# Optimization experiments

Hardware: AMD Instinct MI355X
Metric: run time of the kernel (lower is better)

Reference implementation:

```python
import jax, jax.numpy as jnp
import numpy as np

DEPTH, HEADS, DIM, DH = 6, 3, 3, 128
INNER = HEADS * DH            # 384
M = int(DH * np.log(DH))      # 620 random features (performer_pytorch default)
FF = 4 * DIM                  # 12
EPS = 1e-4


def setup_inputs() -> dict:
    key = jax.random.key(0)
    ks = jax.random.split(key, 12)
    B, N = 8, 4096
    s = 0.1
    return {
        "x": jax.random.normal(ks[0], (B, N, DIM), jnp.float32),
        "Wq": jax.random.normal(ks[1], (DEPTH, DIM, INNER), jnp.float32) * s,
        "Wk": jax.random.normal(ks[2], (DEPTH, DIM, INNER), jnp.float32) * s,
        "Wv": jax.random.normal(ks[3], (DEPTH, DIM, INNER), jnp.float32) * s,
        "Wo": jax.random.normal(ks[4], (DEPTH, INNER, DIM), jnp.float32) * s,
        "bo": jnp.zeros((DEPTH, DIM), jnp.float32),
        "ln1_g": jnp.ones((DEPTH, DIM), jnp.float32),
        "ln1_b": jnp.zeros((DEPTH, DIM), jnp.float32),
        "W1": jax.random.normal(ks[5], (DEPTH, DIM, FF), jnp.float32) * s,
        "b1": jnp.zeros((DEPTH, FF), jnp.float32),
        "W2": jax.random.normal(ks[6], (DEPTH, FF, DIM), jnp.float32) * s,
        "b2": jnp.zeros((DEPTH, DIM), jnp.float32),
        "ln2_g": jnp.ones((DEPTH, DIM), jnp.float32),
        "ln2_b": jnp.zeros((DEPTH, DIM), jnp.float32),
        "proj": jax.random.normal(ks[7], (DEPTH, M, DH), jnp.float32),
        "dec_w": jax.random.normal(ks[8], (DIM, 1), jnp.float32) * s,
        "dec_b": jnp.zeros((1,), jnp.float32),
    }


def layernorm(x, g, b):
    mu = x.mean(-1, keepdims=True)
    var = ((x - mu) ** 2).mean(-1, keepdims=True)
    return (x - mu) * jax.lax.rsqrt(var + 1e-5) * g + b


def softmax_kernel(data, proj, is_query):
    # data: [b,h,n,dh], proj: [m,dh] -> positive random features [b,h,n,m]
    dn = DH ** -0.25                    # data normalizer 1/sqrt(sqrt(d))
    ratio = M ** -0.5
    dd = jnp.einsum('bhnd,md->bhnm', data * dn, proj)
    diag = 0.5 * (dn ** 2) * (data ** 2).sum(-1, keepdims=True)  # [b,h,n,1]
    if is_query:
        mx = jnp.max(dd, axis=-1, keepdims=True)
    else:
        mx = jnp.max(dd, axis=(-1, -2), keepdims=True)
    return ratio * (jnp.exp(dd - diag - mx) + EPS)


def favor_attention(x, Wq, Wk, Wv, Wo, bo, proj):
    b, n, _ = x.shape
    split = lambda t: t.reshape(b, n, HEADS, DH).transpose(0, 2, 1, 3)
    q, k, v = split(x @ Wq), split(x @ Wk), split(x @ Wv)   # [b,h,n,dh]
    qp = softmax_kernel(q, proj, True)    # [b,h,n,m]
    kp = softmax_kernel(k, proj, False)
    k_sum = kp.sum(axis=2)                                   # [b,h,m]
    d_inv = 1.0 / jnp.einsum('bhnm,bhm->bhn', qp, k_sum)
    ctx = jnp.einsum('bhnm,bhnd->bhmd', kp, v)               # [b,h,m,dh]
    out = jnp.einsum('bhnm,bhmd,bhn->bhnd', qp, ctx, d_inv)
    out = out.transpose(0, 2, 1, 3).reshape(b, n, INNER)
    return out @ Wo + bo


def reference(x, Wq, Wk, Wv, Wo, bo, ln1_g, ln1_b, W1, b1, W2, b2, ln2_g, ln2_b, proj, dec_w, dec_b):
    for i in range(DEPTH):
        h = layernorm(x, ln1_g[i], ln1_b[i])
        x = x + favor_attention(h, Wq[i], Wk[i], Wv[i], Wo[i], bo[i], proj[i])
        h = layernorm(x, ln2_g[i], ln2_b[i])
        x = x + (jax.nn.gelu(h @ W1[i] + b1[i], approximate=False) @ W2[i] + b2[i])
    return jax.nn.sigmoid(x @ dec_w + dec_b)
```

## Files before the change

kernel.cpp:

```cpp
#include <hip/hip_runtime.h>
#include <math.h>

#define B_ 8
#define N_ 4096
#define H_ 3
#define DH_ 128
#define INNER_ 384
#define M_ 620
#define MP_ 640
#define DEPTH_ 6
#define BH_ 24

static constexpr float DN_ = 0.29730177875068026f;
static constexpr float RATIO_ = 0.04016096644512494f;
static constexpr float EPS_ = 1e-4f;

typedef __attribute__((ext_vector_type(8))) short short8;
typedef __attribute__((ext_vector_type(4))) float f32x4;

__device__ __forceinline__ short f2bf(float f) {
  union { float f; unsigned u; } x; x.f = f;
  unsigned r = x.u + 0x7FFF + ((x.u >> 16) & 1);
  return (short)(r >> 16);
}
__device__ __forceinline__ float bf2f(short s) {
  union { unsigned u; float f; } x; x.u = ((unsigned)(unsigned short)s) << 16;
  return x.f;
}
__device__ __forceinline__ float4 ldg4(const float* p) { return *(const float4*)p; }

__device__ __forceinline__ unsigned cvtpk(float lo, float hi) {
  unsigned r;
  asm("v_cvt_pk_bf16_f32 %0, %1, %2" : "=v"(r) : "v"(lo), "v"(hi));
  return r;
}

__device__ __forceinline__ void gl2lds(const void* g, void* l) {
  __builtin_amdgcn_global_load_lds(
      (const __attribute__((address_space(1))) void*)g,
      (__attribute__((address_space(3))) void*)l, 16, 0, 0);
}

__device__ __forceinline__ void stage_t256(const char* gbase, char* lds, int w, int l) {
  int row = w * 4 + (l >> 4);
  int col = ((l & 15) * 16) ^ ((row & 7) << 4);
  char* lp = lds + __builtin_amdgcn_readfirstlane(w << 10);
  gl2lds(gbase + row * 256 + col, lp);
}

__device__ __forceinline__ void stage_t64(const char* gbase, size_t growb, char* lds,
                                          int w, int l) {
  int d = w * 16 + (l >> 2);
  int swl = ((((l >> 2) ^ (l >> 4)) & 3) << 4);
  int col = ((l & 3) * 16) ^ swl;
  char* lp = lds + __builtin_amdgcn_readfirstlane(w << 10);
  gl2lds(gbase + (size_t)d * growb + col, lp);
}

__global__ void k_copy(const float* __restrict__ s, float* __restrict__ d, int n) {
  int i = blockIdx.x * 256 + threadIdx.x;
  if (i < n) d[i] = s[i];
}

__global__ void k_projcvt(const float* __restrict__ proj, short* __restrict__ pb) {
  int i = blockIdx.x * 256 + threadIdx.x;
  if (i >= DEPTH_ * MP_ * DH_) return;
  int l = i / (MP_ * DH_);
  int rem = i - l * (MP_ * DH_);
  int m = rem >> 7, d = rem & 127;
  pb[i] = (m < M_) ? f2bf(proj[((size_t)l * M_ + m) * DH_ + d]) : (short)0;
}

__global__ __launch_bounds__(384) void k_ln_qkv(
    const float* __restrict__ x, const float* __restrict__ Wq,
    const float* __restrict__ Wk, const float* __restrict__ Wv,
    const float* __restrict__ g1, const float* __restrict__ b1,
    short* __restrict__ qb, short* __restrict__ kb, short* __restrict__ vtp) {
  __shared__ float xs[96];
  int c = threadIdx.x;
  int token0 = blockIdx.x * 32;
  int b = token0 >> 12, n0 = token0 & 4095;
  if (c < 96) xs[c] = x[(size_t)token0 * 3 + c];
  float wq0 = Wq[c], wq1 = Wq[INNER_ + c], wq2 = Wq[2 * INNER_ + c];
  float wk0 = Wk[c], wk1 = Wk[INNER_ + c], wk2 = Wk[2 * INNER_ + c];
  float wv0 = Wv[c], wv1 = Wv[INNER_ + c], wv2 = Wv[2 * INNER_ + c];
  float G0 = g1[0], G1 = g1[1], G2 = g1[2];
  float B0 = b1[0], B1 = b1[1], B2 = b1[2];
  int hh = c >> 7, dh = c & 127;
  size_t rowbase = ((size_t)(b * H_ + hh) * N_ + n0) * DH_ + dh;
  __syncthreads();
  short8 v8[4];
#pragma unroll
  for (int tt = 0; tt < 32; ++tt) {
    float x0 = xs[tt * 3], x1 = xs[tt * 3 + 1], x2 = xs[tt * 3 + 2];
    float mu = (x0 + x1 + x2) * (1.f / 3.f);
    float d0 = x0 - mu, d1 = x1 - mu, d2 = x2 - mu;
    float rs = rsqrtf((d0 * d0 + d1 * d1 + d2 * d2) * (1.f / 3.f) + 1e-5f);
    float h0 = d0 * rs * G0 + B0;
    float h1 = d1 * rs * G1 + B1;
    float h2 = d2 * rs * G2 + B2;
    qb[rowbase + (size_t)tt * DH_] = f2bf((h0 * wq0 + h1 * wq1 + h2 * wq2) * DN_);
    kb[rowbase + (size_t)tt * DH_] = f2bf((h0 * wk0 + h1 * wk1 + h2 * wk2) * DN_);
    const int p = ((tt >> 2) & 3) * 8 + ((tt >> 4) & 1) * 4 + (tt & 3);
    v8[p >> 3][p & 7] = f2bf(h0 * wv0 + h1 * wv1 + h2 * wv2);
  }
  short* dst = vtp + ((size_t)(b * H_ + hh) * DH_ + dh) * N_ + n0;
  *(short8*)dst = v8[0];
  *(short8*)(dst + 8) = v8[1];
  *(short8*)(dst + 16) = v8[2];
  *(short8*)(dst + 24) = v8[3];
}

__global__ __launch_bounds__(256) void k_dv(
    const short* __restrict__ kb, const short* __restrict__ vtp,
    float* __restrict__ diag_k, float* __restrict__ vsp) {
  __shared__ float red[256];
  int xx = blockIdx.x, bh = blockIdx.y, t = threadIdx.x;
  if (xx < 128) {
    int d = xx;
    const short8* row = (const short8*)(vtp + ((size_t)bh * DH_ + d) * N_);
    short8 a = row[t * 2], b2 = row[t * 2 + 1];
    float s = 0.f;
#pragma unroll
    for (int j = 0; j < 8; ++j) s += bf2f(a[j]) + bf2f(b2[j]);
    red[t] = s;
    __syncthreads();
    for (int st = 128; st; st >>= 1) {
      if (t < st) red[t] += red[t + st];
      __syncthreads();
    }
    if (t == 0) vsp[bh * DH_ + d] = red[0];
  } else {
    int nt = xx - 128;
    int n = t >> 3, seg = t & 7;
    const short* src = kb + ((size_t)bh * N_ + nt * 32 + n) * DH_ + seg * 16;
    short8 a = *(const short8*)src;
    short8 b2 = *(const short8*)(src + 8);
    float s = 0.f;
#pragma unroll
    for (int j = 0; j < 8; ++j) {
      float va = bf2f(a[j]), vb = bf2f(b2[j]);
      s = fmaf(va, va, s);
      s = fmaf(vb, vb, s);
    }
    s += __shfl_down(s, 4);
    s += __shfl_down(s, 2);
    s += __shfl_down(s, 1);
    if (seg == 0) diag_k[(size_t)bh * N_ + nt * 32 + n] = 0.5f * s;
  }
}

__global__ __launch_bounds__(512) void k_kp_ctx(
    const short* __restrict__ kb, const short* __restrict__ vtp,
    const short* __restrict__ pb, const float* __restrict__ diag_k,
    float* __restrict__ Cpart, float* __restrict__ spart,
    float* __restrict__ bmx) {
  int ns = blockIdx.x, mt = blockIdx.y, bh = blockIdx.z;
  __shared__ __align__(16) char Ks[2][16384];
  __shared__ __align__(16) char Vts[2][16384];
  __shared__ float diag_s[1024];
  int t = threadIdx.x, w = t >> 6, l = t & 63, lr = l & 15, lg = l >> 4;
  {
    const float* dbase = diag_k + (size_t)bh * N_ + ns * 1024;
#pragma unroll
    for (int i = 0; i < 2; ++i) diag_s[t + i * 512] = dbase[t + i * 512];
  }
  int m0 = mt * 128 + w * 16;
  short8 bfr[4];
  {
    const short* pr = pb + (size_t)(m0 + lr) * DH_ + lg * 8;
#pragma unroll
    for (int ks = 0; ks < 4; ++ks) bfr[ks] = *(const short8*)(pr + ks * 32);
  }
  const char* kgb = (const char*)(kb + ((size_t)bh * N_ + ns * 1024) * DH_);
  const char* vgb = (const char*)(vtp + (size_t)bh * DH_ * N_ + ns * 1024);
  stage_t256(kgb, Ks[0], w, l);
  stage_t256(kgb + 32 * 256, Ks[0] + 8192, w, l);
  stage_t64(vgb, (size_t)N_ * 2, Vts[0], w, l);
  stage_t64(vgb + 64, (size_t)N_ * 2, Vts[0] + 8192, w, l);
  __syncthreads();
  f32x4 cacc[8];
#pragma unroll
  for (int db = 0; db < 8; ++db) cacc[db] = (f32x4){0.f, 0.f, 0.f, 0.f};
  float ksacc = 0.f;
  float bm = -INFINITY;
  const bool mv = (m0 + lr) < M_;
  int xk = (lr & 7) << 4;
  int xv = ((lr ^ (lr >> 2)) & 3) << 4;
  for (int pc = 0; pc < 16; ++pc) {
    int cur = pc & 1;
    if (pc < 15) {
      const char* kc = kgb + (size_t)(2 * pc + 2) * 32 * 256;
      stage_t256(kc, Ks[cur ^ 1], w, l);
      stage_t256(kc + 32 * 256, Ks[cur ^ 1] + 8192, w, l);
      const char* vc = vgb + (size_t)(2 * pc + 2) * 64;
      stage_t64(vc, (size_t)N_ * 2, Vts[cur ^ 1], w, l);
      stage_t64(vc + 64, (size_t)N_ * 2, Vts[cur ^ 1] + 8192, w, l);
    }
#pragma unroll
    for (int sub = 0; sub < 2; ++sub) {
      const char* KS = Ks[cur] + sub * 8192;
      const char* VS = Vts[cur] + sub * 8192;
      int n0 = (2 * pc + sub) * 32;
      f32x4 dd[2];
      __builtin_amdgcn_s_setprio(1);
#pragma unroll
      for (int nsub = 0; nsub < 2; ++nsub) {
        f32x4 acc = {0.f, 0.f, 0.f, 0.f};
#pragma unroll
        for (int ks = 0; ks < 4; ++ks)
          acc = __builtin_amdgcn_mfma_f32_16x16x32_bf16(
              *(const short8*)(KS + (nsub * 16 + lr) * 256 +
                               ((lg * 16 + ks * 64) ^ xk)),
              bfr[ks], acc, 0, 0, 0);
        dd[nsub] = acc;
      }
      __builtin_amdgcn_s_setprio(0);
      float cm = -INFINITY;
      if (mv) {
#pragma unroll
        for (int nsub = 0; nsub < 2; ++nsub)
#pragma unroll
          for (int rg = 0; rg < 4; ++rg) cm = fmaxf(cm, dd[nsub][rg]);
      }
#pragma unroll
      for (int off = 1; off < 64; off <<= 1) cm = fmaxf(cm, __shfl_xor(cm, off));
      if (cm > bm) {
        float sc = __expf(bm - cm);
        bm = cm;
        ksacc *= sc;
#pragma unroll
        for (int db = 0; db < 8; ++db)
#pragma unroll
          for (int rg = 0; rg < 4; ++rg) cacc[db][rg] *= sc;
      }
      float ev[8];
#pragma unroll
      for (int nsub = 0; nsub < 2; ++nsub)
#pragma unroll
        for (int rg = 0; rg < 4; ++rg) {
          float e = __expf(dd[nsub][rg] - diag_s[n0 + nsub * 16 + 4 * lg + rg] - bm);
          ev[nsub * 4 + rg] = e;
          ksacc += e;
        }
      union { short8 s8; unsigned u[4]; } ea;
#pragma unroll
      for (int i = 0; i < 4; ++i) ea.u[i] = cvtpk(ev[2 * i], ev[2 * i + 1]);
      __builtin_amdgcn_s_setprio(1);
#pragma unroll
      for (int db = 0; db < 8; ++db)
        cacc[db] = __builtin_amdgcn_mfma_f32_16x16x32_bf16(
            ea.s8, *(const short8*)(VS + (db * 16 + lr) * 64 + ((lg * 16) ^ xv)),
            cacc[db], 0, 0, 0);
      __builtin_amdgcn_s_setprio(0);
    }
    __syncthreads();
  }
  float* Cp = Cpart + ((size_t)ns * BH_ + bh) * MP_ * DH_;
#pragma unroll
  for (int db = 0; db < 8; ++db) {
    int d = db * 16 + lr;
#pragma unroll
    for (int rg = 0; rg < 4; ++rg)
      Cp[(size_t)(m0 + 4 * lg + rg) * DH_ + d] = cacc[db][rg];
  }
  ksacc += __shfl_down(ksacc, 32);
  ksacc += __shfl_down(ksacc, 16);
  if (l < 16) spart[((size_t)ns * BH_ + bh) * MP_ + m0 + l] = ksacc;
  if (l == 0) bmx[((size_t)ns * BH_ + bh) * 40 + mt * 8 + w] = bm;
}

__global__ __launch_bounds__(256) void k_fin_ctx(
    const float* __restrict__ Cpart, const float* __restrict__ vsp,
    const float* __restrict__ bmx,
    short* __restrict__ ctxtp, float* __restrict__ cspart) {
  int mt = blockIdx.x, bh = blockIdx.y;
  __shared__ float vsv[128];
  __shared__ short tile[128][40];
  __shared__ float redm[4];
  int t = threadIdx.x;
  if (t < 128) vsv[t] = vsp[bh * DH_ + t] * EPS_;
  float v = -INFINITY;
  if (t < 160) {
    int nsg = t / 40, g = t - nsg * 40;
    v = bmx[((size_t)nsg * BH_ + bh) * 40 + g];
  }
#pragma unroll
  for (int off = 32; off; off >>= 1) v = fmaxf(v, __shfl_xor(v, off));
  if ((t & 63) == 0) redm[t >> 6] = v;
  __syncthreads();
  float mxg = fmaxf(fmaxf(redm[0], redm[1]), fmaxf(redm[2], redm[3]));
  int r = t >> 3, seg = t & 7;
  int d0 = seg * 16;
  int m = mt * 32 + r;
  int p = ((r >> 2) & 3) * 8 + ((r >> 4) & 1) * 4 + (r & 3);
  const size_t ph = (size_t)BH_ * MP_ * DH_;
  const float* c0 = Cpart + (size_t)bh * MP_ * DH_ + (size_t)m * DH_ + d0;
  if (m < M_) {
    int g = m >> 4;
    float sc0 = __expf(bmx[((size_t)0 * BH_ + bh) * 40 + g] - mxg);
    float sc1 = __expf(bmx[((size_t)1 * BH_ + bh) * 40 + g] - mxg);
    float sc2 = __expf(bmx[((size_t)2 * BH_ + bh) * 40 + g] - mxg);
    float sc3 = __expf(bmx[((size_t)3 * BH_ + bh) * 40 + g] - mxg);
#pragma unroll
    for (int j4 = 0; j4 < 4; ++j4) {
      float4 a = ldg4(c0 + j4 * 4);
      float4 b = ldg4(c0 + ph + j4 * 4);
      float4 c = ldg4(c0 + 2 * ph + j4 * 4);
      float4 e = ldg4(c0 + 3 * ph + j4 * 4);
      float vals[4] = {sc0 * a.x + sc1 * b.x + sc2 * c.x + sc3 * e.x,
                       sc0 * a.y + sc1 * b.y + sc2 * c.y + sc3 * e.y,
                       sc0 * a.z + sc1 * b.z + sc2 * c.z + sc3 * e.z,
                       sc0 * a.w + sc1 * b.w + sc2 * c.w + sc3 * e.w};
#pragma unroll
      for (int j = 0; j < 4; ++j) {
        int d = d0 + j4 * 4 + j;
        tile[d][p] = f2bf(RATIO_ * (vals[j] + vsv[d]));
      }
    }
  } else {
#pragma unroll
    for (int j = 0; j < 16; ++j) tile[d0 + j][p] = 0;
  }
  __syncthreads();
  int d = t >> 1, half = t & 1;
  short* dst = ctxtp + ((size_t)bh * DH_ + d) * MP_ + mt * 32 + half * 16;
  short8 s0 = *(const short8*)&tile[d][half * 16];
  short8 s1 = *(const short8*)&tile[d][half * 16 + 8];
  *(short8*)dst = s0;
  *(short8*)(dst + 8) = s1;
  float cs = 0.f;
#pragma unroll
  for (int j = 0; j < 8; ++j) cs += bf2f(s0[j]) + bf2f(s1[j]);
  cs += __shfl_xor(cs, 1);
  if (half == 0) cspart[((size_t)bh * 20 + mt) * DH_ + d] = cs;
}

__global__ __launch_bounds__(128) void k_fin2(
    const float* __restrict__ cspart, const float* __restrict__ spart,
    const float* __restrict__ bmx,
    float* __restrict__ ctxsum, short* __restrict__ ksum_pb,
    float* __restrict__ ksumtot) {
  int bh = blockIdx.x, d = threadIdx.x;
  __shared__ float redm[2];
  float v = -INFINITY;
  for (int i = d; i < 160; i += 128) {
    int nsg = i / 40, g = i - nsg * 40;
    v = fmaxf(v, bmx[((size_t)nsg * BH_ + bh) * 40 + g]);
  }
#pragma unroll
  for (int off = 32; off; off >>= 1) v = fmaxf(v, __shfl_xor(v, off));
  if ((d & 63) == 0) redm[d >> 6] = v;
  float s = 0.f;
#pragma unroll
  for (int mt = 0; mt < 20; ++mt) s += cspart[((size_t)bh * 20 + mt) * DH_ + d];
  ctxsum[bh * DH_ + d] = s;
  __syncthreads();
  float mxg = fmaxf(redm[0], redm[1]);
  __shared__ float red[128];
  float kt = 0.f;
  for (int m = d; m < MP_; m += 128) {
    float ks = 0.f;
    if (m < M_) {
      size_t o = (size_t)bh * MP_ + m;
      size_t sh = (size_t)BH_ * MP_;
      int g = m >> 4;
      float s0 = __expf(bmx[((size_t)0 * BH_ + bh) * 40 + g] - mxg);
      float s1 = __expf(bmx[((size_t)1 * BH_ + bh) * 40 + g] - mxg);
      float s2 = __expf(bmx[((size_t)2 * BH_ + bh) * 40 + g] - mxg);
      float s3 = __expf(bmx[((size_t)3 * BH_ + bh) * 40 + g] - mxg);
      ks = RATIO_ * (s0 * spart[o] + s1 * spart[o + sh] + s2 * spart[o + 2 * sh] +
                     s3 * spart[o + 3 * sh] + EPS_ * (float)N_);
    }
    int r = m & 31;
    int p = ((r >> 2) & 3) * 8 + ((r >> 4) & 1) * 4 + (r & 3);
    ksum_pb[(size_t)bh * MP_ + (m & ~31) + p] = f2bf(ks);
    kt += ks;
  }
  red[d] = kt;
  __syncthreads();
  for (int st = 64; st > 0; st >>= 1) {
    if (d < st) red[d] += red[d + st];
    __syncthreads();
  }
  if (d == 0) ksumtot[bh] = red[0];
}

__global__ __launch_bounds__(512) void k_q_attn(
    const short* __restrict__ qb, const short* __restrict__ pb,
    const short* __restrict__ ctxtp, const short* __restrict__ ksum_pb,
    const float* __restrict__ ctxsum, const float* __restrict__ ksumtot,
    float* __restrict__ o) {
  int nt = blockIdx.x, bh = blockIdx.y;
  __shared__ __align__(16) char Pj[2][8192];
  __shared__ __align__(16) char Ct[2][8192];
  __shared__ __align__(16) short kslp[MP_];
  int t = threadIdx.x, w = t >> 6, l = t & 63, lr = l & 15, lg = l >> 4;
  if (t < MP_ / 8)
    ((short8*)kslp)[t] = ((const short8*)(ksum_pb + (size_t)bh * MP_))[t];
  const short* qr = qb + ((size_t)bh * N_ + nt * 128 + w * 16 + lr) * DH_ + lg * 8;
  short8 qfr[4];
#pragma unroll
  for (int ks = 0; ks < 4; ++ks) qfr[ks] = *(const short8*)(qr + ks * 32);
  float dq;
  {
    float s2 = 0.f;
#pragma unroll
    for (int ks = 0; ks < 4; ++ks)
#pragma unroll
      for (int j = 0; j < 8; ++j) {
        float v = bf2f(qfr[ks][j]);
        s2 = fmaf(v, v, s2);
      }
    s2 += __shfl_xor(s2, 16);
    s2 += __shfl_xor(s2, 32);
    dq = 0.5f * s2;
  }
  const char* cgb = (const char*)(ctxtp + (size_t)bh * DH_ * MP_);
  stage_t256((const char*)pb, Pj[0], w, l);
  stage_t64(cgb, (size_t)MP_ * 2, Ct[0], w, l);
  __syncthreads();
  f32x4 cacc[8];
#pragma unroll
  for (int db = 0; db < 8; ++db) cacc[db] = (f32x4){0.f, 0.f, 0.f, 0.f};
  f32x4 dacc = {0.f, 0.f, 0.f, 0.f};
  float om = -INFINITY;
  int xk = (lr & 7) << 4;
  int xv = ((lr ^ (lr >> 2)) & 3) << 4;
  for (int mc = 0; mc < 20; ++mc) {
    int cur = mc & 1;
    if (mc < 19) {
      stage_t256((const char*)(pb + (size_t)(mc + 1) * 32 * DH_), Pj[cur ^ 1], w, l);
      stage_t64(cgb + (size_t)(mc + 1) * 64, (size_t)MP_ * 2, Ct[cur ^ 1], w, l);
    }
    int m0 = mc * 32;
    f32x4 qk[2];
    __builtin_amdgcn_s_setprio(1);
#pragma unroll
    for (int ms = 0; ms < 2; ++ms) {
      f32x4 acc = {0.f, 0.f, 0.f, 0.f};
#pragma unroll
      for (int ks = 0; ks < 4; ++ks)
        acc = __builtin_amdgcn_mfma_f32_16x16x32_bf16(
            *(const short8*)(Pj[cur] + (ms * 16 + lr) * 256 +
                             ((lg * 16 + ks * 64) ^ xk)),
            qfr[ks], acc, 0, 0, 0);
      qk[ms] = acc;
    }
    __builtin_amdgcn_s_setprio(0);
    float cm = -INFINITY;
#pragma unroll
    for (int ms = 0; ms < 2; ++ms)
#pragma unroll
      for (int rg = 0; rg < 4; ++rg) {
        int mg = m0 + ms * 16 + 4 * lg + rg;
        if (mg < M_) cm = fmaxf(cm, qk[ms][rg]);
      }
    cm = fmaxf(cm, __shfl_xor(cm, 16));
    cm = fmaxf(cm, __shfl_xor(cm, 32));
    if (__any(cm > om)) {
      float nm = fmaxf(om, cm);
      float sc = __expf(om - nm);
      om = nm;
      float scr[4];
#pragma unroll
      for (int rg = 0; rg < 4; ++rg) scr[rg] = __shfl(sc, 4 * lg + rg);
#pragma unroll
      for (int rg = 0; rg < 4; ++rg) dacc[rg] *= scr[rg];
#pragma unroll
      for (int db = 0; db < 8; ++db)
#pragma unroll
        for (int rg = 0; rg < 4; ++rg) cacc[db][rg] *= scr[rg];
    }
    float dqm = dq + om;
    float ev[8];
#pragma unroll
    for (int ms = 0; ms < 2; ++ms)
#pragma unroll
      for (int rg = 0; rg < 4; ++rg)
        ev[ms * 4 + rg] = __expf(qk[ms][rg] - dqm);
    union { short8 s8; unsigned u[4]; } ea;
#pragma unroll
    for (int i = 0; i < 4; ++i) ea.u[i] = cvtpk(ev[2 * i], ev[2 * i + 1]);
    __builtin_amdgcn_s_setprio(1);
    dacc = __builtin_amdgcn_mfma_f32_16x16x32_bf16(
        ea.s8, *(const short8*)&kslp[m0 + lg * 8], dacc, 0, 0, 0);
#pragma unroll
    for (int db = 0; db < 8; ++db)
      cacc[db] = __builtin_amdgcn_mfma_f32_16x16x32_bf16(
          ea.s8, *(const short8*)(Ct[cur] + (db * 16 + lr) * 64 + ((lg * 16) ^ xv)),
          cacc[db], 0, 0, 0);
    __builtin_amdgcn_s_setprio(0);
    __syncthreads();
  }
  float kst = ksumtot[bh];
  float dinv[4];
#pragma unroll
  for (int rg = 0; rg < 4; ++rg)
    dinv[rg] = 1.f / (RATIO_ * (dacc[rg] + EPS_ * kst));
  float* ob = o + ((size_t)bh * N_ + nt * 128 + w * 16) * DH_;
#pragma unroll
  for (int db = 0; db < 8; ++db) {
    int d = db * 16 + lr;
    float cs = ctxsum[bh * DH_ + d] * EPS_;
#pragma unroll
    for (int rg = 0; rg < 4; ++rg)
      ob[(size_t)(4 * lg + rg) * DH_ + d] = RATIO_ * (cacc[db][rg] + cs) * dinv[rg];
  }
}

__global__ __launch_bounds__(256) void k_wo_ffn(
    const float* __restrict__ attn, const float* __restrict__ Wo,
    const float* __restrict__ bo, const float* __restrict__ g2,
    const float* __restrict__ be2, const float* __restrict__ W1,
    const float* __restrict__ bf1, const float* __restrict__ W2,
    const float* __restrict__ bf2, float* __restrict__ x) {
  __shared__ float wols[INNER_ * 3];
  __shared__ float bos[3];
  __shared__ float acc3[4][8][3];
  int t = threadIdx.x;
  for (int i = t; i < INNER_ * 3; i += 256) wols[i] = Wo[i];
  if (t < 3) bos[t] = bo[t];
  __syncthreads();
  int w = t >> 6, l = t & 63;
  int base = (blockIdx.x * 4 + w) * 8;
#pragma unroll
  for (int tt = 0; tt < 8; ++tt) {
    int token = base + tt;
    int b = token >> 12, n = token & 4095;
    float p0 = 0.f, p1 = 0.f, p2 = 0.f;
#pragma unroll
    for (int s = 0; s < 6; ++s) {
      int inner = l + 64 * s;
      int h = inner >> 7, dh = inner & 127;
      float a = attn[(((size_t)(b * H_ + h)) * N_ + n) * DH_ + dh];
      p0 = fmaf(a, wols[inner * 3 + 0], p0);
      p1 = fmaf(a, wols[inner * 3 + 1], p1);
      p2 = fmaf(a, wols[inner * 3 + 2], p2);
    }
#pragma unroll
    for (int off = 32; off; off >>= 1) {
      p0 += __shfl_down(p0, off);
      p1 += __shfl_down(p1, off);
      p2 += __shfl_down(p2, off);
    }
    if (l == 0) {
      acc3[w][tt][0] = p0 + bos[0];
      acc3[w][tt][1] = p1 + bos[1];
      acc3[w][tt][2] = p2 + bos[2];
    }
  }
  __syncthreads();
  if (l < 8) {
    int token = base + l;
    float x0 = x[(size_t)token * 3 + 0] + acc3[w][l][0];
    float x1 = x[(size_t)token * 3 + 1] + acc3[w][l][1];
    float x2 = x[(size_t)token * 3 + 2] + acc3[w][l][2];
    float mu = (x0 + x1 + x2) * (1.f / 3.f);
    float d0 = x0 - mu, d1 = x1 - mu, d2 = x2 - mu;
    float rs = rsqrtf((d0 * d0 + d1 * d1 + d2 * d2) * (1.f / 3.f) + 1e-5f);
    float h0 = d0 * rs * g2[0] + be2[0];
    float h1 = d1 * rs * g2[1] + be2[1];
    float h2 = d2 * rs * g2[2] + be2[2];
    float y0 = x0 + bf2[0], y1 = x1 + bf2[1], y2 = x2 + bf2[2];
#pragma unroll
    for (int tt = 0; tt < 12; ++tt) {
      float f = h0 * W1[tt] + h1 * W1[12 + tt] + h2 * W1[24 + tt] + bf1[tt];
      float g = 0.5f * f * (1.f + erff(f * 0.70710678118654752f));
      y0 += g * W2[tt * 3 + 0];
      y1 += g * W2[tt * 3 + 1];
      y2 += g * W2[tt * 3 + 2];
    }
    x[(size_t)token * 3 + 0] = y0;
    x[(size_t)token * 3 + 1] = y1;
    x[(size_t)token * 3 + 2] = y2;
  }
}

__global__ void k_decode(const float* __restrict__ x, const float* __restrict__ dw,
                         const float* __restrict__ db, float* __restrict__ out) {
  int t = blockIdx.x * 256 + threadIdx.x;
  if (t < B_ * N_) {
    float l = x[(size_t)t * 3 + 0] * dw[0] + x[(size_t)t * 3 + 1] * dw[1] +
              x[(size_t)t * 3 + 2] * dw[2] + db[0];
    out[t] = 1.f / (1.f + expf(-l));
  }
}

extern "C" void kernel_launch(void* const* d_in, const int* in_sizes, int n_in,
                              void* d_out, int out_size, void* d_ws, size_t ws_size,
                              hipStream_t stream) {
  const float* x_in = (const float*)d_in[0];
  const float* Wq = (const float*)d_in[1];
  const float* Wk = (const float*)d_in[2];
  const float* Wv = (const float*)d_in[3];
  const float* Wo = (const float*)d_in[4];
  const float* bo = (const float*)d_in[5];
  const float* ln1g = (const float*)d_in[6];
  const float* ln1b = (const float*)d_in[7];
  const float* W1 = (const float*)d_in[8];
  const float* b1 = (const float*)d_in[9];
  const float* W2 = (const float*)d_in[10];
  const float* b2 = (const float*)d_in[11];
  const float* ln2g = (const float*)d_in[12];
  const float* ln2b = (const float*)d_in[13];
  const float* proj = (const float*)d_in[14];
  const float* dec_w = (const float*)d_in[15];
  const float* dec_b = (const float*)d_in[16];

  const size_t XB = (size_t)B_ * N_ * 3;
  const size_t QKV = (size_t)BH_ * N_ * DH_;
  const size_t CTX = (size_t)BH_ * MP_ * DH_;
  const size_t SS = (size_t)BH_ * MP_;

  char* p = (char*)d_ws;
  auto alloc = [&](size_t bytes) {
    char* r = p;
    p += (bytes + 255) & ~(size_t)255;
    return r;
  };
  float* xbuf = (float*)alloc(XB * 4);
  short* qb = (short*)alloc(QKV * 2);
  short* kb = (short*)alloc(QKV * 2);
  float* diag_k = (float*)alloc((size_t)BH_ * N_ * 4);
  short* pb = (short*)alloc((size_t)DEPTH_ * MP_ * DH_ * 2);
  short* vtp = (short*)alloc(QKV * 2);
  short* ctxtp = (short*)alloc(CTX * 2);
  float* o = (float*)alloc(QKV * 4);
  float* Cpart = o;
  float* spart = (float*)alloc(4 * SS * 4);
  float* cspart = (float*)alloc((size_t)BH_ * 20 * DH_ * 4);
  short* ksum_pb = (short*)alloc(SS * 2);
  float* vsp = (float*)alloc((size_t)BH_ * DH_ * 4);
  float* ctxsum = (float*)alloc((size_t)BH_ * DH_ * 4);
  float* ksumtot = (float*)alloc(BH_ * 4);
  float* bmx = (float*)alloc((size_t)4 * BH_ * 40 * 4);

  k_copy<<<(XB + 255) / 256, 256, 0, stream>>>(x_in, xbuf, (int)XB);
  k_projcvt<<<(DEPTH_ * MP_ * DH_ + 255) / 256, 256, 0, stream>>>(proj, pb);

  for (int i = 0; i < DEPTH_; ++i) {
    const short* pbL = pb + (size_t)i * MP_ * DH_;
    k_ln_qkv<<<B_ * N_ / 32, 384, 0, stream>>>(xbuf, Wq + (size_t)i * 3 * INNER_,
                                               Wk + (size_t)i * 3 * INNER_,
                                               Wv + (size_t)i * 3 * INNER_,
                                               ln1g + i * 3, ln1b + i * 3,
                                               qb, kb, vtp);
    k_dv<<<dim3(256, BH_), 256, 0, stream>>>(kb, vtp, diag_k, vsp);
    k_kp_ctx<<<dim3(4, 5, BH_), 512, 0, stream>>>(kb, vtp, pbL, diag_k,
                                                  Cpart, spart, bmx);
    k_fin_ctx<<<dim3(20, BH_), 256, 0, stream>>>(Cpart, vsp, bmx, ctxtp, cspart);
    k_fin2<<<BH_, 128, 0, stream>>>(cspart, spart, bmx, ctxsum, ksum_pb, ksumtot);
    k_q_attn<<<dim3(32, BH_), 512, 0, stream>>>(qb, pbL, ctxtp, ksum_pb,
                                                ctxsum, ksumtot, o);
    k_wo_ffn<<<B_ * N_ / 32, 256, 0, stream>>>(o, Wo + (size_t)i * INNER_ * 3,
                                               bo + i * 3, ln2g + i * 3, ln2b + i * 3,
                                               W1 + (size_t)i * 36, b1 + (size_t)i * 12,
                                               W2 + (size_t)i * 36, b2 + i * 3, xbuf);
  }
  k_decode<<<(B_ * N_ + 255) / 256, 256, 0, stream>>>(xbuf, dec_w, dec_b, (float*)d_out);
}
```

Before: 1.044 ms.

## Fuse k-norm and v-sum reductions into QKV kernel; store attention output as bf16

Removes the separate k_dv kernel by computing the per-token squared norm of k (via wave shuffles and shared memory) and per-tile partial sums of v inside k_ln_qkv. The v partial sums are reduced in k_fin_ctx. The attention output buffer o becomes bf16 instead of fp32, halving its write and read traffic between k_q_attn and k_wo_ffn, and Cpart gets its own allocation that o aliases. This trades one kernel launch and a full re-read of k and v for extra shuffle work in the QKV kernel and some loss of precision in the attention output.

```diff
diff --git a/kernel.cpp b/kernel.cpp
--- a/kernel.cpp
+++ b/kernel.cpp
@@ -75,8 +75,10 @@
     const float* __restrict__ x, const float* __restrict__ Wq,
     const float* __restrict__ Wk, const float* __restrict__ Wv,
     const float* __restrict__ g1, const float* __restrict__ b1,
-    short* __restrict__ qb, short* __restrict__ kb, short* __restrict__ vtp) {
+    short* __restrict__ qb, short* __restrict__ kb, short* __restrict__ vtp,
+    float* __restrict__ diag_k, float* __restrict__ vsppart) {
   __shared__ float xs[96];
+  __shared__ float wred[6][32];
   int c = threadIdx.x;
   int token0 = blockIdx.x * 32;
   int b = token0 >> 12, n0 = token0 & 4095;
@@ -87,9 +89,11 @@
   float G0 = g1[0], G1 = g1[1], G2 = g1[2];
   float B0 = b1[0], B1 = b1[1], B2 = b1[2];
   int hh = c >> 7, dh = c & 127;
+  int w = c >> 6;
   size_t rowbase = ((size_t)(b * H_ + hh) * N_ + n0) * DH_ + dh;
   __syncthreads();
   short8 v8[4];
+  float vsum_acc = 0.f;
 #pragma unroll
   for (int tt = 0; tt < 32; ++tt) {
     float x0 = xs[tt * 3], x1 = xs[tt * 3 + 1], x2 = xs[tt * 3 + 2];
@@ -100,53 +104,29 @@
     float h1 = d1 * rs * G1 + B1;
     float h2 = d2 * rs * G2 + B2;
     qb[rowbase + (size_t)tt * DH_] = f2bf((h0 * wq0 + h1 * wq1 + h2 * wq2) * DN_);
-    kb[rowbase + (size_t)tt * DH_] = f2bf((h0 * wk0 + h1 * wk1 + h2 * wk2) * DN_);
+    short kbs = f2bf((h0 * wk0 + h1 * wk1 + h2 * wk2) * DN_);
+    kb[rowbase + (size_t)tt * DH_] = kbs;
+    float kvr = bf2f(kbs);
+    float kk = kvr * kvr;
+#pragma unroll
+    for (int off = 32; off; off >>= 1) kk += __shfl_xor(kk, off);
+    if ((c & 63) == 0) wred[w][tt] = kk;
+    short vbs = f2bf(h0 * wv0 + h1 * wv1 + h2 * wv2);
+    vsum_acc += bf2f(vbs);
     const int p = ((tt >> 2) & 3) * 8 + ((tt >> 4) & 1) * 4 + (tt & 3);
-    v8[p >> 3][p & 7] = f2bf(h0 * wv0 + h1 * wv1 + h2 * wv2);
+    v8[p >> 3][p & 7] = vbs;
   }
   short* dst = vtp + ((size_t)(b * H_ + hh) * DH_ + dh) * N_ + n0;
   *(short8*)dst = v8[0];
   *(short8*)(dst + 8) = v8[1];
   *(short8*)(dst + 16) = v8[2];
   *(short8*)(dst + 24) = v8[3];
-}
-
-__global__ __launch_bounds__(256) void k_dv(
-    const short* __restrict__ kb, const short* __restrict__ vtp,
-    float* __restrict__ diag_k, float* __restrict__ vsp) {
-  __shared__ float red[256];
-  int xx = blockIdx.x, bh = blockIdx.y, t = threadIdx.x;
-  if (xx < 128) {
-    int d = xx;
-    const short8* row = (const short8*)(vtp + ((size_t)bh * DH_ + d) * N_);
-    short8 a = row[t * 2], b2 = row[t * 2 + 1];
-    float s = 0.f;
-#pragma unroll
-    for (int j = 0; j < 8; ++j) s += bf2f(a[j]) + bf2f(b2[j]);
-    red[t] = s;
-    __syncthreads();
-    for (int st = 128; st; st >>= 1) {
-      if (t < st) red[t] += red[t + st];
-      __syncthreads();
-    }
-    if (t == 0) vsp[bh * DH_ + d] = red[0];
-  } else {
-    int nt = xx - 128;
-    int n = t >> 3, seg = t & 7;
-    const short* src = kb + ((size_t)bh * N_ + nt * 32 + n) * DH_ + seg * 16;
-    short8 a = *(const short8*)src;
-    short8 b2 = *(const short8*)(src + 8);
-    float s = 0.f;
-#pragma unroll
-    for (int j = 0; j < 8; ++j) {
-      float va = bf2f(a[j]), vb = bf2f(b2[j]);
-      s = fmaf(va, va, s);
-      s = fmaf(vb, vb, s);
-    }
-    s += __shfl_down(s, 4);
-    s += __shfl_down(s, 2);
-    s += __shfl_down(s, 1);
-    if (seg == 0) diag_k[(size_t)bh * N_ + nt * 32 + n] = 0.5f * s;
+  vsppart[((size_t)(b * H_ + hh) * DH_ + dh) * 128 + (n0 >> 5)] = vsum_acc;
+  __syncthreads();
+  if (c < 96) {
+    int h2 = c >> 5, tt = c & 31;
+    diag_k[(size_t)(b * H_ + h2) * N_ + n0 + tt] =
+        0.5f * (wred[2 * h2][tt] + wred[2 * h2 + 1][tt]);
   }
 }
 
@@ -271,7 +251,7 @@
 }
 
 __global__ __launch_bounds__(256) void k_fin_ctx(
-    const float* __restrict__ Cpart, const float* __restrict__ vsp,
+    const float* __restrict__ Cpart, const float* __restrict__ vsppart,
     const float* __restrict__ bmx,
     short* __restrict__ ctxtp, float* __restrict__ cspart) {
   int mt = blockIdx.x, bh = blockIdx.y;
@@ -279,7 +259,13 @@
   __shared__ short tile[128][40];
   __shared__ float redm[4];
   int t = threadIdx.x;
-  if (t < 128) vsv[t] = vsp[bh * DH_ + t] * EPS_;
+  if (t < 128) {
+    const float* vp = vsppart + ((size_t)bh * DH_ + t) * 128;
+    float s = 0.f;
+#pragma unroll 8
+    for (int i = 0; i < 128; ++i) s += vp[i];
+    vsv[t] = s * EPS_;
+  }
   float v = -INFINITY;
   if (t < 160) {
     int nsg = t / 40, g = t - nsg * 40;
@@ -390,7 +376,7 @@
     const short* __restrict__ qb, const short* __restrict__ pb,
     const short* __restrict__ ctxtp, const short* __restrict__ ksum_pb,
     const float* __restrict__ ctxsum, const float* __restrict__ ksumtot,
-    float* __restrict__ o) {
+    short* __restrict__ o) {
   int nt = blockIdx.x, bh = blockIdx.y;
   __shared__ __align__(16) char Pj[2][8192];
   __shared__ __align__(16) char Ct[2][8192];
@@ -498,19 +484,20 @@
 #pragma unroll
   for (int rg = 0; rg < 4; ++rg)
     dinv[rg] = 1.f / (RATIO_ * (dacc[rg] + EPS_ * kst));
-  float* ob = o + ((size_t)bh * N_ + nt * 128 + w * 16) * DH_;
+  short* ob = o + ((size_t)bh * N_ + nt * 128 + w * 16) * DH_;
 #pragma unroll
   for (int db = 0; db < 8; ++db) {
     int d = db * 16 + lr;
     float cs = ctxsum[bh * DH_ + d] * EPS_;
 #pragma unroll
     for (int rg = 0; rg < 4; ++rg)
-      ob[(size_t)(4 * lg + rg) * DH_ + d] = RATIO_ * (cacc[db][rg] + cs) * dinv[rg];
+      ob[(size_t)(4 * lg + rg) * DH_ + d] =
+          f2bf(RATIO_ * (cacc[db][rg] + cs) * dinv[rg]);
   }
 }
 
 __global__ __launch_bounds__(256) void k_wo_ffn(
-    const float* __restrict__ attn, const float* __restrict__ Wo,
+    const short* __restrict__ attn, const float* __restrict__ Wo,
     const float* __restrict__ bo, const float* __restrict__ g2,
     const float* __restrict__ be2, const float* __restrict__ W1,
     const float* __restrict__ bf1, const float* __restrict__ W2,
@@ -533,7 +520,7 @@
     for (int s = 0; s < 6; ++s) {
       int inner = l + 64 * s;
       int h = inner >> 7, dh = inner & 127;
-      float a = attn[(((size_t)(b * H_ + h)) * N_ + n) * DH_ + dh];
+      float a = bf2f(attn[(((size_t)(b * H_ + h)) * N_ + n) * DH_ + dh]);
       p0 = fmaf(a, wols[inner * 3 + 0], p0);
       p1 = fmaf(a, wols[inner * 3 + 1], p1);
       p2 = fmaf(a, wols[inner * 3 + 2], p2);
@@ -626,12 +613,12 @@
   short* pb = (short*)alloc((size_t)DEPTH_ * MP_ * DH_ * 2);
   short* vtp = (short*)alloc(QKV * 2);
   short* ctxtp = (short*)alloc(CTX * 2);
-  float* o = (float*)alloc(QKV * 4);
-  float* Cpart = o;
+  float* Cpart = (float*)alloc((size_t)4 * BH_ * MP_ * DH_ * 4);
+  short* o = (short*)Cpart;
   float* spart = (float*)alloc(4 * SS * 4);
   float* cspart = (float*)alloc((size_t)BH_ * 20 * DH_ * 4);
   short* ksum_pb = (short*)alloc(SS * 2);
-  float* vsp = (float*)alloc((size_t)BH_ * DH_ * 4);
+  float* vsppart = (float*)alloc((size_t)BH_ * DH_ * 128 * 4);
   float* ctxsum = (float*)alloc((size_t)BH_ * DH_ * 4);
   float* ksumtot = (float*)alloc(BH_ * 4);
   float* bmx = (float*)alloc((size_t)4 * BH_ * 40 * 4);
@@ -645,11 +632,10 @@
                                                Wk + (size_t)i * 3 * INNER_,
                                                Wv + (size_t)i * 3 * INNER_,
                                                ln1g + i * 3, ln1b + i * 3,
-                                               qb, kb, vtp);
-    k_dv<<<dim3(256, BH_), 256, 0, stream>>>(kb, vtp, diag_k, vsp);
+                                               qb, kb, vtp, diag_k, vsppart);
     k_kp_ctx<<<dim3(4, 5, BH_), 512, 0, stream>>>(kb, vtp, pbL, diag_k,
                                                   Cpart, spart, bmx);
-    k_fin_ctx<<<dim3(20, BH_), 256, 0, stream>>>(Cpart, vsp, bmx, ctxtp, cspart);
+    k_fin_ctx<<<dim3(20, BH_), 256, 0, stream>>>(Cpart, vsppart, bmx, ctxtp, cspart);
     k_fin2<<<BH_, 128, 0, stream>>>(cspart, spart, bmx, ctxsum, ksum_pb, ksumtot);
     k_q_attn<<<dim3(32, BH_), 512, 0, stream>>>(qb, pbL, ctxtp, ksum_pb,
                                                 ctxsum, ksumtot, o);
```

New measurement: 1.155 ms, median of 2. +10.6%, slower.
